# Kernel optimization log

Measured on AMD Instinct MI355X. Metric: run time of the kernel, lower is better.

Reference implementation:

```python
import jax, jax.numpy as jnp
import numpy as np

B, D, E, K = 65536, 1024, 8, 2

def setup_inputs() -> dict:
    key = jax.random.key(0)
    k1, k2, k3, k4, k5 = jax.random.split(key, 5)
    s = 1.0 / np.sqrt(D)
    return {
        "x": jax.random.normal(k1, (B, D), dtype=jnp.float32),
        "gate_w": jax.random.uniform(k2, (E, D), dtype=jnp.float32, minval=-s, maxval=s),
        "gate_b": jax.random.uniform(k3, (E,), dtype=jnp.float32, minval=-s, maxval=s),
        "expert_w": jax.random.uniform(k4, (E, D), dtype=jnp.float32, minval=-s, maxval=s),  # row e = weight of expert e's Linear(D,1)
        "expert_b": jax.random.uniform(k5, (E,), dtype=jnp.float32, minval=-s, maxval=s),
        "k": K,
    }

def reference(x, gate_w, gate_b, expert_w, expert_b, k):
    # gate: [B, E]
    gate_scores = jax.nn.softmax(x @ gate_w.T + gate_b, axis=1)
    E_ = gate_w.shape[0]
    if k < E_:
        topk_vals, topk_idx = jax.lax.top_k(gate_scores, k)  # [B, k]
        rows = jnp.arange(x.shape[0])[:, None]
        gate_scores = jnp.zeros_like(gate_scores).at[rows, topk_idx].set(topk_vals)
    # per-expert Linear(D,1) stacked: [B, E]
    expert_outputs = x @ expert_w.T + expert_b
    # weighted sum over experts -> [B, 1]
    moe_output = jnp.sum(gate_scores * expert_outputs, axis=1, keepdims=True)
    return moe_output
```

## Files before the change

kernel.cpp:

```cpp
#include <hip/hip_runtime.h>


#define BLOCK 512
#define DD 1024
#define EE 8
#define ROWS_PER_WAVE 16
#define ROWS_PER_BLOCK ((BLOCK / 64) * ROWS_PER_WAVE)

__global__ __launch_bounds__(BLOCK, 4) void moe_gate_kernel(
    const float* __restrict__ x,
    const float* __restrict__ gate_w,
    const float* __restrict__ gate_b,
    const float* __restrict__ expert_w,
    const float* __restrict__ expert_b,
    const int* __restrict__ kp,
    float* __restrict__ out)
{
    __shared__ float wlds[2 * EE * DD];

    const int tid = threadIdx.x;

    {
        const float4* g4 = (const float4*)gate_w;
        const float4* e4 = (const float4*)expert_w;
        float4* w4 = (float4*)wlds;
#pragma unroll
        for (int i = 0; i < (EE * DD / 4) / BLOCK; ++i) {
            int idx = i * BLOCK + tid;
            w4[idx] = g4[idx];
            w4[EE * DD / 4 + idx] = e4[idx];
        }
    }
    __syncthreads();

    const int lane = tid & 63;
    const int wave = tid >> 6;
    const int s = lane >> 3;
    const int j = lane & 7;

    const int row0 = blockIdx.x * ROWS_PER_BLOCK + wave * ROWS_PER_WAVE + 2 * s;
    const float* xr0 = x + (size_t)row0 * DD + j * 4;
    const float* xr1 = xr0 + DD;

    const float* wb = wlds + j * 4;

    float acc0[16], acc1[16];
#pragma unroll
    for (int i = 0; i < 16; ++i) { acc0[i] = 0.f; acc1[i] = 0.f; }

    auto step = [&](int c, const float4& x0, const float4& x1) {
        const int wc = c * 32;
#pragma unroll
        for (int o = 0; o < 16; ++o) {
            float4 w = *(const float4*)(wb + o * DD + wc);
            acc0[o] = fmaf(x0.x, w.x, acc0[o]);
            acc1[o] = fmaf(x1.x, w.x, acc1[o]);
            acc0[o] = fmaf(x0.y, w.y, acc0[o]);
            acc1[o] = fmaf(x1.y, w.y, acc1[o]);
            acc0[o] = fmaf(x0.z, w.z, acc0[o]);
            acc1[o] = fmaf(x1.z, w.z, acc1[o]);
            acc0[o] = fmaf(x0.w, w.w, acc0[o]);
            acc1[o] = fmaf(x1.w, w.w, acc1[o]);
        }
    };

    float4 a0 = *(const float4*)(xr0);
    float4 a1 = *(const float4*)(xr1);
#pragma unroll 1
    for (int c = 0; c < DD / 32 - 1; ++c) {
        float4 b0 = *(const float4*)(xr0 + (c + 1) * 32);
        float4 b1 = *(const float4*)(xr1 + (c + 1) * 32);
        step(c, a0, a1);
        a0 = b0; a1 = b1;
    }
    step(DD / 32 - 1, a0, a1);

#pragma unroll
    for (int i = 0; i < 16; ++i) {
        acc0[i] += __shfl_xor(acc0[i], 1);
        acc1[i] += __shfl_xor(acc1[i], 1);
        acc0[i] += __shfl_xor(acc0[i], 2);
        acc1[i] += __shfl_xor(acc1[i], 2);
        acc0[i] += __shfl_xor(acc0[i], 4);
        acc1[i] += __shfl_xor(acc1[i], 4);
    }

    if (j == 0) {
        const int k = *kp;
#pragma unroll
        for (int r = 0; r < 2; ++r) {
            const float* acc = r ? acc1 : acc0;
            float gl[8], eo[8], p[8];
#pragma unroll
            for (int e = 0; e < EE; ++e) {
                gl[e] = acc[e] + gate_b[e];
                eo[e] = acc[8 + e] + expert_b[e];
            }
            float m = gl[0];
#pragma unroll
            for (int e = 1; e < EE; ++e) m = fmaxf(m, gl[e]);
            float Z = 0.f;
#pragma unroll
            for (int e = 0; e < EE; ++e) { p[e] = __expf(gl[e] - m); Z += p[e]; }

            float res = 0.f;
            if (k >= EE) {
#pragma unroll
                for (int e = 0; e < EE; ++e) res += p[e] * eo[e];
            } else {
                float pv[8];
#pragma unroll
                for (int e = 0; e < EE; ++e) pv[e] = p[e];
                for (int t = 0; t < k; ++t) {
                    float bv = pv[0];
#pragma unroll
                    for (int e = 1; e < EE; ++e) bv = fmaxf(bv, pv[e]);
                    float sel = 0.f;
                    bool found = false;
#pragma unroll
                    for (int e = 0; e < EE; ++e) {
                        bool is = (!found) && (pv[e] == bv);
                        sel = is ? eo[e] : sel;
                        pv[e] = is ? -1.f : pv[e];
                        found = found || is;
                    }
                    res += bv * sel;
                }
            }
            out[row0 + r] = res / Z;
        }
    }
}

extern "C" void kernel_launch(void* const* d_in, const int* in_sizes, int n_in,
                              void* d_out, int out_size, void* d_ws, size_t ws_size,
                              hipStream_t stream) {
    const float* x  = (const float*)d_in[0];
    const float* gw = (const float*)d_in[1];
    const float* gb = (const float*)d_in[2];
    const float* ew = (const float*)d_in[3];
    const float* eb = (const float*)d_in[4];
    const int*   kp = (const int*)d_in[5];
    float* out = (float*)d_out;

    const int B = out_size;
    dim3 grid(B / ROWS_PER_BLOCK), block(BLOCK);
    moe_gate_kernel<<<grid, block, 0, stream>>>(x, gw, gb, ew, eb, kp, out);
}
```

Before: 50.11 us.

## Process four rows per lane group to double LDS weight reuse

Reorganizes each wave into four 16-lane groups that each handle four rows, reading 64-column chunks instead of 32. Each weight vector loaded from LDS now feeds four rows of FMAs instead of two, cutting LDS read traffic per FMA. The cost is double the accumulator registers plus an extra shuffle-reduction stage, which raises register pressure under the existing launch bounds.

```diff
diff --git a/kernel.cpp b/kernel.cpp
--- a/kernel.cpp
+++ b/kernel.cpp
@@ -6,6 +6,10 @@
 #define EE 8
 #define ROWS_PER_WAVE 16
 #define ROWS_PER_BLOCK ((BLOCK / 64) * ROWS_PER_WAVE)
+#define CHUNK 64
+#define NCHUNK (DD / CHUNK)
+
+typedef float vf4 __attribute__((ext_vector_type(4)));
 
 __global__ __launch_bounds__(BLOCK, 4) void moe_gate_kernel(
     const float* __restrict__ x,
@@ -35,66 +39,68 @@
 
     const int lane = tid & 63;
     const int wave = tid >> 6;
-    const int s = lane >> 3;
-    const int j = lane & 7;
+    const int s = lane >> 4;
+    const int j = lane & 15;
 
-    const int row0 = blockIdx.x * ROWS_PER_BLOCK + wave * ROWS_PER_WAVE + 2 * s;
-    const float* xr0 = x + (size_t)row0 * DD + j * 4;
-    const float* xr1 = xr0 + DD;
+    const int row0 = blockIdx.x * ROWS_PER_BLOCK + wave * ROWS_PER_WAVE + 4 * s;
+    const float* xr = x + (size_t)row0 * DD + j * 4;
 
     const float* wb = wlds + j * 4;
 
-    float acc0[16], acc1[16];
+    float acc[4][16];
 #pragma unroll
-    for (int i = 0; i < 16; ++i) { acc0[i] = 0.f; acc1[i] = 0.f; }
+    for (int r = 0; r < 4; ++r)
+#pragma unroll
+        for (int o = 0; o < 16; ++o) acc[r][o] = 0.f;
 
-    auto step = [&](int c, const float4& x0, const float4& x1) {
-        const int wc = c * 32;
+    auto step = [&](int c, const vf4 xv[4]) {
+        const int wc = c * CHUNK;
 #pragma unroll
         for (int o = 0; o < 16; ++o) {
-            float4 w = *(const float4*)(wb + o * DD + wc);
-            acc0[o] = fmaf(x0.x, w.x, acc0[o]);
-            acc1[o] = fmaf(x1.x, w.x, acc1[o]);
-            acc0[o] = fmaf(x0.y, w.y, acc0[o]);
-            acc1[o] = fmaf(x1.y, w.y, acc1[o]);
-            acc0[o] = fmaf(x0.z, w.z, acc0[o]);
-            acc1[o] = fmaf(x1.z, w.z, acc1[o]);
-            acc0[o] = fmaf(x0.w, w.w, acc0[o]);
-            acc1[o] = fmaf(x1.w, w.w, acc1[o]);
+            vf4 w = *(const vf4*)(wb + o * DD + wc);
+#pragma unroll
+            for (int r = 0; r < 4; ++r) {
+                acc[r][o] = fmaf(xv[r].x, w.x, acc[r][o]);
+                acc[r][o] = fmaf(xv[r].y, w.y, acc[r][o]);
+                acc[r][o] = fmaf(xv[r].z, w.z, acc[r][o]);
+                acc[r][o] = fmaf(xv[r].w, w.w, acc[r][o]);
+            }
         }
     };
 
-    float4 a0 = *(const float4*)(xr0);
-    float4 a1 = *(const float4*)(xr1);
+    vf4 cur[4], nxt[4];
+#pragma unroll
+    for (int r = 0; r < 4; ++r) cur[r] = *(const vf4*)(xr + (size_t)r * DD);
 #pragma unroll 1
-    for (int c = 0; c < DD / 32 - 1; ++c) {
-        float4 b0 = *(const float4*)(xr0 + (c + 1) * 32);
-        float4 b1 = *(const float4*)(xr1 + (c + 1) * 32);
-        step(c, a0, a1);
-        a0 = b0; a1 = b1;
+    for (int c = 0; c < NCHUNK - 1; ++c) {
+#pragma unroll
+        for (int r = 0; r < 4; ++r)
+            nxt[r] = *(const vf4*)(xr + (size_t)r * DD + (c + 1) * CHUNK);
+        step(c, cur);
+#pragma unroll
+        for (int r = 0; r < 4; ++r) cur[r] = nxt[r];
     }
-    step(DD / 32 - 1, a0, a1);
+    step(NCHUNK - 1, cur);
 
 #pragma unroll
-    for (int i = 0; i < 16; ++i) {
-        acc0[i] += __shfl_xor(acc0[i], 1);
-        acc1[i] += __shfl_xor(acc1[i], 1);
-        acc0[i] += __shfl_xor(acc0[i], 2);
-        acc1[i] += __shfl_xor(acc1[i], 2);
-        acc0[i] += __shfl_xor(acc0[i], 4);
-        acc1[i] += __shfl_xor(acc1[i], 4);
-    }
+    for (int r = 0; r < 4; ++r)
+#pragma unroll
+        for (int o = 0; o < 16; ++o) {
+            acc[r][o] += __shfl_xor(acc[r][o], 1);
+            acc[r][o] += __shfl_xor(acc[r][o], 2);
+            acc[r][o] += __shfl_xor(acc[r][o], 4);
+            acc[r][o] += __shfl_xor(acc[r][o], 8);
+        }
 
     if (j == 0) {
         const int k = *kp;
 #pragma unroll
-        for (int r = 0; r < 2; ++r) {
-            const float* acc = r ? acc1 : acc0;
+        for (int r = 0; r < 4; ++r) {
             float gl[8], eo[8], p[8];
 #pragma unroll
             for (int e = 0; e < EE; ++e) {
-                gl[e] = acc[e] + gate_b[e];
-                eo[e] = acc[8 + e] + expert_b[e];
+                gl[e] = acc[r][e] + gate_b[e];
+                eo[e] = acc[r][8 + e] + expert_b[e];
             }
             float m = gl[0];
 #pragma unroll
```

Measured after the change: 59.58 us. 18.9% more time.
